# Performance work log

Measured on AMD Instinct MI355X. Metric: run time of the kernel, lower is better.

## Reference

```python
import jax, jax.numpy as jnp
import numpy as np
from jax.ops import segment_sum

N_V = 50000   # vertices
N_E = 10000   # hyperedges
N_P = 800000  # incidence pairs
D_IN = 256
D_OUT = 256
NEG_SLOPE = 0.01


def setup_inputs() -> dict:
    key = jax.random.key(0)
    k1, k2, k3, k4, k5 = jax.random.split(key, 5)
    X = jax.random.normal(k1, (N_V, D_IN), dtype=jnp.float32)
    W = jax.random.normal(k2, (D_IN, D_OUT), dtype=jnp.float32) * (1.0 / np.sqrt(D_IN))
    b = jax.random.normal(k3, (D_OUT,), dtype=jnp.float32) * 0.01
    v_idx = jax.random.randint(k4, (N_P,), 0, N_V, dtype=jnp.int32)
    e_idx = jax.random.randint(k5, (N_P,), 0, N_E, dtype=jnp.int32)
    return {"X": X, "W": W, "b": b, "v_idx": v_idx, "e_idx": e_idx,
            "num_hyperedges": N_E}


def _mean_scatter(msg, idx, num_segments):
    # segment mean with count clamped to >=1 (empty segments -> 0)
    s = segment_sum(msg, idx, num_segments=num_segments)
    cnt = segment_sum(jnp.ones((msg.shape[0],), msg.dtype), idx,
                      num_segments=num_segments)
    return s / jnp.maximum(cnt, 1.0)[:, None]


def reference(X, W, b, v_idx, e_idx, num_hyperedges):
    # theta: linear projection  [N_V, D_OUT]
    H = X @ W + b
    # v2e mean: hyperedge features from member vertices
    e_feat = _mean_scatter(H[v_idx], e_idx, num_hyperedges)   # [N_E, D_OUT]
    # e2v mean: vertex features from incident hyperedges
    v_feat = _mean_scatter(e_feat[e_idx], v_idx, X.shape[0])  # [N_V, D_OUT]
    # leaky relu, default negative slope 0.01
    return jnp.where(v_feat >= 0, v_feat, NEG_SLOPE * v_feat)
```

## Files before the change

### kernel.cpp

```cpp
#include <hip/hip_runtime.h>

#define D 256
#define NEG_SLOPE 0.01f
#define E_PAD 192
#define V_PAD 64
#define EB 32
#define VB 64
#define NBE 313
#define NBV 782
#define CAP_E 3328
#define CAP_V 1536
#define CHUNK 4096
#define NS 8
#define DS 32
#define NSE 2
#define DSE 128

__device__ __forceinline__ unsigned short f2bf(float f) {
    union { float f; unsigned u; } x; x.f = f;
    unsigned r = x.u + 0x7fffu + ((x.u >> 16) & 1u);
    return (unsigned short)(r >> 16);
}
__device__ __forceinline__ void acc8(float* acc, uint4 g) {
    union { unsigned u; float f; } t;
    t.u = g.x << 16;         acc[0] += t.f;
    t.u = g.x & 0xffff0000u; acc[1] += t.f;
    t.u = g.y << 16;         acc[2] += t.f;
    t.u = g.y & 0xffff0000u; acc[3] += t.f;
    t.u = g.z << 16;         acc[4] += t.f;
    t.u = g.z & 0xffff0000u; acc[5] += t.f;
    t.u = g.w << 16;         acc[6] += t.f;
    t.u = g.w & 0xffff0000u; acc[7] += t.f;
}

__global__ __launch_bounds__(256) void prep_kernel(
        const float* __restrict__ X, unsigned short* __restrict__ Xhs,
        const int* __restrict__ v_idx, const int* __restrict__ e_idx,
        int* __restrict__ bc_e, int* __restrict__ bc_v,
        unsigned* __restrict__ pe, unsigned* __restrict__ pv,
        int n_v, int n_p, int gp) {
    __shared__ int he[NBE], hv[NBV], beb[NBE], bvb[NBV];
    const int tid = threadIdx.x;
    if ((int)blockIdx.x < gp) {
        const int base = (int)blockIdx.x * CHUNK;
        for (int i = tid; i < NBE; i += 256) he[i] = 0;
        for (int i = tid; i < NBV; i += 256) hv[i] = 0;
        __syncthreads();
        #pragma unroll 4
        for (int r = 0; r < CHUNK / 256; ++r) {
            int p = base + r * 256 + tid;
            if (p < n_p) {
                atomicAdd(&he[e_idx[p] >> 5], 1);
                atomicAdd(&hv[v_idx[p] >> 6], 1);
            }
        }
        __syncthreads();
        for (int b = tid; b < NBE; b += 256) {
            int c = he[b];
            beb[b] = c ? atomicAdd(&bc_e[b], c) : 0;
            he[b] = 0;
        }
        for (int b = tid; b < NBV; b += 256) {
            int c = hv[b];
            bvb[b] = c ? atomicAdd(&bc_v[b], c) : 0;
            hv[b] = 0;
        }
        __syncthreads();
        #pragma unroll 4
        for (int r = 0; r < CHUNK / 256; ++r) {
            int p = base + r * 256 + tid;
            if (p < n_p) {
                int e = e_idx[p], v = v_idx[p];
                int b1 = e >> 5;
                int s1 = beb[b1] + atomicAdd(&he[b1], 1);
                if (s1 < CAP_E) pe[(size_t)b1 * CAP_E + s1] = (unsigned)v | ((unsigned)e << 16);
                int b2 = v >> 6;
                int s2 = bvb[b2] + atomicAdd(&hv[b2], 1);
                if (s2 < CAP_V) pv[(size_t)b2 * CAP_V + s2] = (unsigned)e | ((unsigned)v << 16);
            }
        }
    } else {
        int i = ((int)blockIdx.x - gp) * 256 + tid;
        if (i >= n_v * 64) return;
        int v = i >> 6;
        int d4 = (i & 63) * 4;
        float4 val = *(const float4*)(X + (size_t)v * D + d4);
        ushort4 h;
        h.x = f2bf(val.x); h.y = f2bf(val.y); h.z = f2bf(val.z); h.w = f2bf(val.w);
        int s = d4 >> 5, wd = d4 & 31;
        *(ushort4*)(Xhs + (size_t)s * n_v * DS + (size_t)v * DS + wd) = h;
    }
}

__global__ __launch_bounds__(256) void build_kernel(
        const unsigned* __restrict__ pe, const unsigned* __restrict__ pv,
        const int* __restrict__ bc_e, const int* __restrict__ bc_v,
        unsigned short* __restrict__ e_adj, int* __restrict__ e_fill,
        unsigned short* __restrict__ v_adj, int* __restrict__ v_fill,
        int n_e, int n_v) {
    __shared__ unsigned short adj[EB * E_PAD];
    __shared__ int cnt[VB];
    const int tid = threadIdx.x;
    if ((int)blockIdx.x < NBE) {
        const int b = blockIdx.x;
        const int e0 = b * EB;
        int m = n_e - e0; if (m > EB) m = EB;
        for (int i = tid; i < EB; i += 256) cnt[i] = 0;
        __syncthreads();
        int total = bc_e[b]; if (total > CAP_E) total = CAP_E;
        for (int i = tid; i < total; i += 256) {
            unsigned p = pe[(size_t)b * CAP_E + i];
            int v = (int)(p & 0xFFFFu);
            int el = (int)(p >> 16) - e0;
            int s = atomicAdd(&cnt[el], 1);
            if (s < E_PAD) adj[el * E_PAD + s] = (unsigned short)v;
        }
        __syncthreads();
        unsigned* gout = (unsigned*)(e_adj + (size_t)e0 * E_PAD);
        const unsigned* lin = (const unsigned*)adj;
        int words = m * E_PAD / 2;
        for (int j = tid; j < words; j += 256) gout[j] = lin[j];
        for (int el = tid; el < m; el += 256) {
            int c = cnt[el]; if (c > E_PAD) c = E_PAD;
            e_fill[e0 + el] = c;
        }
    } else {
        const int b = (int)blockIdx.x - NBE;
        const int v0 = b * VB;
        int m = n_v - v0; if (m > VB) m = VB;
        for (int i = tid; i < VB; i += 256) cnt[i] = 0;
        __syncthreads();
        int total = bc_v[b]; if (total > CAP_V) total = CAP_V;
        for (int i = tid; i < total; i += 256) {
            unsigned p = pv[(size_t)b * CAP_V + i];
            int e = (int)(p & 0xFFFFu);
            int vl = (int)(p >> 16) - v0;
            int s = atomicAdd(&cnt[vl], 1);
            if (s < V_PAD) adj[vl * V_PAD + s] = (unsigned short)e;
        }
        __syncthreads();
        unsigned* gout = (unsigned*)(v_adj + (size_t)v0 * V_PAD);
        const unsigned* lin = (const unsigned*)adj;
        int words = m * V_PAD / 2;
        for (int j = tid; j < words; j += 256) gout[j] = lin[j];
        for (int vl = tid; vl < m; vl += 256) {
            int c = cnt[vl]; if (c > V_PAD) c = V_PAD;
            v_fill[v0 + vl] = c;
        }
    }
}

__global__ __launch_bounds__(256) void v2e_kernel(
        const unsigned short* __restrict__ Xhs, const int* __restrict__ e_fill,
        const unsigned short* __restrict__ e_adj, float* __restrict__ Xagg,
        int n_e, int n_v) {
    const int s    = blockIdx.x;
    const int eg   = threadIdx.x >> 4;
    const int l16  = threadIdx.x & 15;
    const int ph   = l16 >> 2;
    const int sub  = l16 & 3;
    const int e    = blockIdx.y * 16 + eg;
    if (e >= n_e) return;
    const unsigned short* tab = Xhs + (size_t)s * n_v * DS + (sub << 3);
    const unsigned short* adj = e_adj + (size_t)e * E_PAD;
    int cnt = e_fill[e]; if (cnt > E_PAD) cnt = E_PAD;
    float acc[8] = {};
    int i = ph * 4;
    for (; i + 4 <= cnt; i += 16) {
        ushort4 A = *(const ushort4*)(adj + i);
        uint4 g0 = *(const uint4*)(tab + (size_t)A.x * DS);
        uint4 g1 = *(const uint4*)(tab + (size_t)A.y * DS);
        uint4 g2 = *(const uint4*)(tab + (size_t)A.z * DS);
        uint4 g3 = *(const uint4*)(tab + (size_t)A.w * DS);
        acc8(acc, g0); acc8(acc, g1); acc8(acc, g2); acc8(acc, g3);
    }
    for (int j = i; j < cnt; ++j) {
        uint4 g = *(const uint4*)(tab + (size_t)adj[j] * DS);
        acc8(acc, g);
    }
    #pragma unroll
    for (int k = 0; k < 8; ++k) {
        acc[k] += __shfl_xor(acc[k], 4);
        acc[k] += __shfl_xor(acc[k], 8);
    }
    if (ph == 0) {
        int c = cnt < 1 ? 1 : cnt;
        float inv = 1.0f / (float)c;
        float4 o0, o1;
        o0.x = acc[0] * inv; o0.y = acc[1] * inv; o0.z = acc[2] * inv; o0.w = acc[3] * inv;
        o1.x = acc[4] * inv; o1.y = acc[5] * inv; o1.z = acc[6] * inv; o1.w = acc[7] * inv;
        float* orow = Xagg + (size_t)e * D + s * DS + (sub << 3);
        *(float4*)(orow)     = o0;
        *(float4*)(orow + 4) = o1;
    }
}

#define BM 64
#define BN 64
#define BK 64
#define SAK 68
#define SBN 68

__global__ __launch_bounds__(256) void gemm_kernel(
        const float* __restrict__ A, const float* __restrict__ B,
        const float* __restrict__ bias, const int* __restrict__ e_cnt,
        unsigned short* __restrict__ Ehs, int M) {
    __shared__ float As[BM * SAK];
    __shared__ float Bs[BK * SBN];
    const int tid = threadIdx.x;
    const int tx = tid & 15, ty = tid >> 4;
    const int m0 = blockIdx.y * BM;
    const int n0 = blockIdx.x * BN;

    float acc[4][4] = {};

    for (int k0 = 0; k0 < D; k0 += BK) {
        #pragma unroll
        for (int r = 0; r < 4; ++r) {
            int l  = (tid + r * 256) * 4;
            int am = l >> 6;
            int ak = l & 63;
            int grow = m0 + am;
            float4 v = make_float4(0.f, 0.f, 0.f, 0.f);
            if (grow < M) v = *(const float4*)(A + (size_t)grow * D + k0 + ak);
            *(float4*)(&As[am * SAK + ak]) = v;
        }
        #pragma unroll
        for (int r = 0; r < 4; ++r) {
            int l  = (tid + r * 256) * 4;
            int bk = l >> 6;
            int bn = l & 63;
            float4 v = *(const float4*)(B + (size_t)(k0 + bk) * D + n0 + bn);
            *(float4*)(&Bs[bk * SBN + bn]) = v;
        }
        __syncthreads();

        #pragma unroll 8
        for (int kk = 0; kk < BK; ++kk) {
            float a0 = As[(ty * 4 + 0) * SAK + kk];
            float a1 = As[(ty * 4 + 1) * SAK + kk];
            float a2 = As[(ty * 4 + 2) * SAK + kk];
            float a3 = As[(ty * 4 + 3) * SAK + kk];
            float4 bv = *(const float4*)(Bs + kk * SBN + tx * 4);
            acc[0][0] += a0 * bv.x; acc[0][1] += a0 * bv.y; acc[0][2] += a0 * bv.z; acc[0][3] += a0 * bv.w;
            acc[1][0] += a1 * bv.x; acc[1][1] += a1 * bv.y; acc[1][2] += a1 * bv.z; acc[1][3] += a1 * bv.w;
            acc[2][0] += a2 * bv.x; acc[2][1] += a2 * bv.y; acc[2][2] += a2 * bv.z; acc[2][3] += a2 * bv.w;
            acc[3][0] += a3 * bv.x; acc[3][1] += a3 * bv.y; acc[3][2] += a3 * bv.z; acc[3][3] += a3 * bv.w;
        }
        __syncthreads();
    }

    float4 bb = *(const float4*)(bias + n0 + tx * 4);
    const int dcol = n0 + tx * 4;
    const int ss = dcol >> 7, wd = dcol & 127;
    #pragma unroll
    for (int i = 0; i < 4; ++i) {
        int row = m0 + ty * 4 + i;
        if (row < M) {
            bool nonempty = e_cnt[row] > 0;
            ushort4 o;
            o.x = f2bf(nonempty ? acc[i][0] + bb.x : 0.f);
            o.y = f2bf(nonempty ? acc[i][1] + bb.y : 0.f);
            o.z = f2bf(nonempty ? acc[i][2] + bb.z : 0.f);
            o.w = f2bf(nonempty ? acc[i][3] + bb.w : 0.f);
            *(ushort4*)(Ehs + (size_t)ss * M * DSE + (size_t)row * DSE + wd) = o;
        }
    }
}

__global__ __launch_bounds__(256) void e2v_kernel(
        const unsigned short* __restrict__ Ehs, const unsigned short* __restrict__ v_adj,
        const int* __restrict__ v_fill, float* __restrict__ out, int n_v, int n_e) {
    const int s   = blockIdx.x;
    const int grp = threadIdx.x >> 4;
    const int sub = threadIdx.x & 15;
    const int v   = blockIdx.y * 16 + grp;
    if (v >= n_v) return;
    const unsigned short* tab = Ehs + (size_t)s * n_e * DSE + (sub << 3);
    const unsigned short* a   = v_adj + (size_t)v * V_PAD;
    int c = v_fill[v]; if (c > V_PAD) c = V_PAD;
    float acc[8] = {};
    int i = 0;
    for (; i + 8 <= c; i += 8) {
        ushort4 E0 = *(const ushort4*)(a + i);
        ushort4 E1 = *(const ushort4*)(a + i + 4);
        uint4 g0 = *(const uint4*)(tab + (size_t)E0.x * DSE);
        uint4 g1 = *(const uint4*)(tab + (size_t)E0.y * DSE);
        uint4 g2 = *(const uint4*)(tab + (size_t)E0.z * DSE);
        uint4 g3 = *(const uint4*)(tab + (size_t)E0.w * DSE);
        uint4 g4 = *(const uint4*)(tab + (size_t)E1.x * DSE);
        uint4 g5 = *(const uint4*)(tab + (size_t)E1.y * DSE);
        uint4 g6 = *(const uint4*)(tab + (size_t)E1.z * DSE);
        uint4 g7 = *(const uint4*)(tab + (size_t)E1.w * DSE);
        acc8(acc, g0); acc8(acc, g1); acc8(acc, g2); acc8(acc, g3);
        acc8(acc, g4); acc8(acc, g5); acc8(acc, g6); acc8(acc, g7);
    }
    for (; i < c; ++i) {
        uint4 g = *(const uint4*)(tab + (size_t)a[i] * DSE);
        acc8(acc, g);
    }
    int cc = c < 1 ? 1 : c;
    float inv = 1.0f / (float)cc;
    float4 o0, o1;
    #pragma unroll
    for (int k = 0; k < 8; ++k) acc[k] *= inv;
    o0.x = acc[0] >= 0.f ? acc[0] : NEG_SLOPE * acc[0];
    o0.y = acc[1] >= 0.f ? acc[1] : NEG_SLOPE * acc[1];
    o0.z = acc[2] >= 0.f ? acc[2] : NEG_SLOPE * acc[2];
    o0.w = acc[3] >= 0.f ? acc[3] : NEG_SLOPE * acc[3];
    o1.x = acc[4] >= 0.f ? acc[4] : NEG_SLOPE * acc[4];
    o1.y = acc[5] >= 0.f ? acc[5] : NEG_SLOPE * acc[5];
    o1.z = acc[6] >= 0.f ? acc[6] : NEG_SLOPE * acc[6];
    o1.w = acc[7] >= 0.f ? acc[7] : NEG_SLOPE * acc[7];
    float* orow = out + (size_t)v * D + s * DSE + (sub << 3);
    *(float4*)(orow)     = o0;
    *(float4*)(orow + 4) = o1;
}

extern "C" void kernel_launch(void* const* d_in, const int* in_sizes, int n_in,
                              void* d_out, int out_size, void* d_ws, size_t ws_size,
                              hipStream_t stream) {
    const float* X    = (const float*)d_in[0];
    const float* W    = (const float*)d_in[1];
    const float* bias = (const float*)d_in[2];
    const int* v_idx  = (const int*)d_in[3];
    const int* e_idx  = (const int*)d_in[4];
    const int n_v = in_sizes[0] / D;
    const int n_p = in_sizes[3];
    const int n_e = 10000;

    char* w = (char*)d_ws;
    size_t off = 0;
    auto alloc = [&](size_t bytes) -> void* {
        void* p = w + off;
        off = (off + bytes + 255) & ~(size_t)255;
        return p;
    };
    unsigned short* Xhs = (unsigned short*)alloc((size_t)NS * n_v * DS * sizeof(unsigned short));
    float* Xagg         = (float*)alloc((size_t)n_e * D * sizeof(float));
    unsigned short* Ehs = (unsigned short*)alloc((size_t)n_e * D * sizeof(unsigned short));
    unsigned short* e_adj = (unsigned short*)alloc((size_t)n_e * E_PAD * sizeof(unsigned short));
    unsigned short* v_adj = (unsigned short*)alloc((size_t)n_v * V_PAD * sizeof(unsigned short));
    unsigned* pe   = (unsigned*)alloc((size_t)NBE * CAP_E * sizeof(unsigned));
    unsigned* pv   = (unsigned*)alloc((size_t)NBV * CAP_V * sizeof(unsigned));
    int* fills     = (int*)alloc((size_t)(n_e + n_v) * sizeof(int));
    int* e_fill = fills;
    int* v_fill = fills + n_e;
    int* bc        = (int*)alloc((size_t)(NBE + NBV) * sizeof(int));
    int* bc_e = bc;
    int* bc_v = bc + NBE;

    hipMemsetAsync(bc, 0, (size_t)(NBE + NBV) * sizeof(int), stream);

    int gp = (n_p + CHUNK - 1) / CHUNK;
    int gc = (n_v * 64 + 255) / 256;
    prep_kernel<<<gp + gc, 256, 0, stream>>>(X, Xhs, v_idx, e_idx,
                                             bc_e, bc_v, pe, pv, n_v, n_p, gp);

    build_kernel<<<NBE + NBV, 256, 0, stream>>>(pe, pv, bc_e, bc_v,
                                                e_adj, e_fill, v_adj, v_fill,
                                                n_e, n_v);

    dim3 vgrid(NS, (n_e + 15) / 16);
    v2e_kernel<<<vgrid, 256, 0, stream>>>(Xhs, e_fill, e_adj, Xagg, n_e, n_v);

    dim3 ggrid(D / BN, (n_e + BM - 1) / BM);
    gemm_kernel<<<ggrid, 256, 0, stream>>>(Xagg, W, bias, e_fill, Ehs, n_e);

    dim3 egrid(NSE, (n_v + 15) / 16);
    e2v_kernel<<<egrid, 256, 0, stream>>>(Ehs, v_adj, v_fill, (float*)d_out, n_v, n_e);
}
```

Measured before the change: 235.8 us.

## Replace global atomic bucket offsets with histogram+scan pipeline and alias workspace buffers

Splits the single prep kernel into a per-chunk histogram kernel, a per-bucket exclusive scan kernel, and a scatter kernel that reads its precomputed offsets. This drops the global atomicAdd on bucket counters and the memset, and makes bucket placement deterministic. Workspace is also aliased: pe shares memory with Xagg/Ehs and pv is placed in the output buffer, which shrinks the footprint and may improve cache locality. In exchange it adds two extra kernel launches, and the chunk count gp is silently clamped to 256, which would drop data if n_p grew.

```diff
diff --git a/kernel.cpp b/kernel.cpp
--- a/kernel.cpp
+++ b/kernel.cpp
@@ -8,9 +8,11 @@
 #define VB 64
 #define NBE 313
 #define NBV 782
+#define NBT (NBE + NBV)
 #define CAP_E 3328
 #define CAP_V 1536
 #define CHUNK 4096
+#define CR (CHUNK/256)
 #define NS 8
 #define DS 32
 #define NSE 2
@@ -33,49 +35,71 @@
     t.u = g.w & 0xffff0000u; acc[7] += t.f;
 }
 
-__global__ __launch_bounds__(256) void prep_kernel(
+__global__ __launch_bounds__(256) void hist_kernel(
+        const int* __restrict__ v_idx, const int* __restrict__ e_idx,
+        int* __restrict__ offs, int n_p, int gp) {
+    __shared__ int he[NBE], hv[NBV];
+    const int tid = threadIdx.x, blk = blockIdx.x;
+    for (int i = tid; i < NBE; i += 256) he[i] = 0;
+    for (int i = tid; i < NBV; i += 256) hv[i] = 0;
+    __syncthreads();
+    const int base = blk * CHUNK;
+    #pragma unroll 4
+    for (int r = 0; r < CR; ++r) {
+        int p = base + r * 256 + tid;
+        if (p < n_p) {
+            atomicAdd(&he[e_idx[p] >> 5], 1);
+            atomicAdd(&hv[v_idx[p] >> 6], 1);
+        }
+    }
+    __syncthreads();
+    const int g1 = gp + 1;
+    for (int b = tid; b < NBE; b += 256) offs[(size_t)b * g1 + blk] = he[b];
+    for (int b = tid; b < NBV; b += 256) offs[(size_t)(NBE + b) * g1 + blk] = hv[b];
+}
+
+__global__ __launch_bounds__(256) void scan_kernel(int* __restrict__ offs, int gp) {
+    __shared__ int sa[256], sb[256];
+    const int tid = threadIdx.x;
+    int* row = offs + (size_t)blockIdx.x * (gp + 1);
+    sa[tid] = tid < gp ? row[tid] : 0;
+    __syncthreads();
+    int *src = sa, *dst = sb;
+    for (int s = 1; s < 256; s <<= 1) {
+        int t = src[tid] + (tid >= s ? src[tid - s] : 0);
+        dst[tid] = t;
+        __syncthreads();
+        int* tmp = src; src = dst; dst = tmp;
+    }
+    if (tid < gp) row[tid] = tid ? src[tid - 1] : 0;
+    if (tid == 0) row[gp] = src[gp - 1];
+}
+
+__global__ __launch_bounds__(256) void scatter_kernel(
         const float* __restrict__ X, unsigned short* __restrict__ Xhs,
         const int* __restrict__ v_idx, const int* __restrict__ e_idx,
-        int* __restrict__ bc_e, int* __restrict__ bc_v,
+        const int* __restrict__ offs,
         unsigned* __restrict__ pe, unsigned* __restrict__ pv,
         int n_v, int n_p, int gp) {
-    __shared__ int he[NBE], hv[NBV], beb[NBE], bvb[NBV];
+    __shared__ int oe[NBE], ov[NBV], he[NBE], hv[NBV];
     const int tid = threadIdx.x;
     if ((int)blockIdx.x < gp) {
-        const int base = (int)blockIdx.x * CHUNK;
-        for (int i = tid; i < NBE; i += 256) he[i] = 0;
-        for (int i = tid; i < NBV; i += 256) hv[i] = 0;
-        __syncthreads();
+        const int blk = blockIdx.x;
+        const int g1 = gp + 1;
+        for (int b = tid; b < NBE; b += 256) { oe[b] = offs[(size_t)b * g1 + blk]; he[b] = 0; }
+        for (int b = tid; b < NBV; b += 256) { ov[b] = offs[(size_t)(NBE + b) * g1 + blk]; hv[b] = 0; }
+        __syncthreads();
+        const int base = blk * CHUNK;
         #pragma unroll 4
-        for (int r = 0; r < CHUNK / 256; ++r) {
-            int p = base + r * 256 + tid;
-            if (p < n_p) {
-                atomicAdd(&he[e_idx[p] >> 5], 1);
-                atomicAdd(&hv[v_idx[p] >> 6], 1);
-            }
-        }
-        __syncthreads();
-        for (int b = tid; b < NBE; b += 256) {
-            int c = he[b];
-            beb[b] = c ? atomicAdd(&bc_e[b], c) : 0;
-            he[b] = 0;
-        }
-        for (int b = tid; b < NBV; b += 256) {
-            int c = hv[b];
-            bvb[b] = c ? atomicAdd(&bc_v[b], c) : 0;
-            hv[b] = 0;
-        }
-        __syncthreads();
-        #pragma unroll 4
-        for (int r = 0; r < CHUNK / 256; ++r) {
+        for (int r = 0; r < CR; ++r) {
             int p = base + r * 256 + tid;
             if (p < n_p) {
                 int e = e_idx[p], v = v_idx[p];
                 int b1 = e >> 5;
-                int s1 = beb[b1] + atomicAdd(&he[b1], 1);
+                int s1 = oe[b1] + atomicAdd(&he[b1], 1);
                 if (s1 < CAP_E) pe[(size_t)b1 * CAP_E + s1] = (unsigned)v | ((unsigned)e << 16);
                 int b2 = v >> 6;
-                int s2 = bvb[b2] + atomicAdd(&hv[b2], 1);
+                int s2 = ov[b2] + atomicAdd(&hv[b2], 1);
                 if (s2 < CAP_V) pv[(size_t)b2 * CAP_V + s2] = (unsigned)e | ((unsigned)v << 16);
             }
         }
@@ -94,20 +118,21 @@
 
 __global__ __launch_bounds__(256) void build_kernel(
         const unsigned* __restrict__ pe, const unsigned* __restrict__ pv,
-        const int* __restrict__ bc_e, const int* __restrict__ bc_v,
+        const int* __restrict__ offs,
         unsigned short* __restrict__ e_adj, int* __restrict__ e_fill,
         unsigned short* __restrict__ v_adj, int* __restrict__ v_fill,
-        int n_e, int n_v) {
+        int n_e, int n_v, int gp) {
     __shared__ unsigned short adj[EB * E_PAD];
     __shared__ int cnt[VB];
     const int tid = threadIdx.x;
+    const int g1 = gp + 1;
     if ((int)blockIdx.x < NBE) {
         const int b = blockIdx.x;
         const int e0 = b * EB;
         int m = n_e - e0; if (m > EB) m = EB;
         for (int i = tid; i < EB; i += 256) cnt[i] = 0;
         __syncthreads();
-        int total = bc_e[b]; if (total > CAP_E) total = CAP_E;
+        int total = offs[(size_t)b * g1 + gp]; if (total > CAP_E) total = CAP_E;
         for (int i = tid; i < total; i += 256) {
             unsigned p = pe[(size_t)b * CAP_E + i];
             int v = (int)(p & 0xFFFFu);
@@ -130,7 +155,7 @@
         int m = n_v - v0; if (m > VB) m = VB;
         for (int i = tid; i < VB; i += 256) cnt[i] = 0;
         __syncthreads();
-        int total = bc_v[b]; if (total > CAP_V) total = CAP_V;
+        int total = offs[(size_t)(NBE + b) * g1 + gp]; if (total > CAP_V) total = CAP_V;
         for (int i = tid; i < total; i += 256) {
             unsigned p = pv[(size_t)b * CAP_V + i];
             int e = (int)(p & 0xFFFFu);
@@ -329,6 +354,9 @@
     const int n_p = in_sizes[3];
     const int n_e = 10000;
 
+    int gp = (n_p + CHUNK - 1) / CHUNK;
+    if (gp > 256) gp = 256;
+
     char* w = (char*)d_ws;
     size_t off = 0;
     auto alloc = [&](size_t bytes) -> void* {
@@ -337,29 +365,33 @@
         return p;
     };
     unsigned short* Xhs = (unsigned short*)alloc((size_t)NS * n_v * DS * sizeof(unsigned short));
-    float* Xagg         = (float*)alloc((size_t)n_e * D * sizeof(float));
-    unsigned short* Ehs = (unsigned short*)alloc((size_t)n_e * D * sizeof(unsigned short));
+    size_t pe_bytes  = (size_t)NBE * CAP_E * sizeof(unsigned);
+    size_t agg_bytes = (size_t)n_e * D * sizeof(float);
+    size_t ehs_bytes = (size_t)n_e * D * sizeof(unsigned short);
+    size_t uni_bytes = pe_bytes > agg_bytes + ehs_bytes ? pe_bytes : agg_bytes + ehs_bytes;
+    char* uni = (char*)alloc(uni_bytes);
+    unsigned* pe        = (unsigned*)uni;
+    float* Xagg         = (float*)uni;
+    unsigned short* Ehs = (unsigned short*)(uni + agg_bytes);
+    unsigned* pv        = (unsigned*)d_out;
     unsigned short* e_adj = (unsigned short*)alloc((size_t)n_e * E_PAD * sizeof(unsigned short));
     unsigned short* v_adj = (unsigned short*)alloc((size_t)n_v * V_PAD * sizeof(unsigned short));
-    unsigned* pe   = (unsigned*)alloc((size_t)NBE * CAP_E * sizeof(unsigned));
-    unsigned* pv   = (unsigned*)alloc((size_t)NBV * CAP_V * sizeof(unsigned));
+    int* offs      = (int*)alloc((size_t)NBT * (gp + 1) * sizeof(int));
     int* fills     = (int*)alloc((size_t)(n_e + n_v) * sizeof(int));
     int* e_fill = fills;
     int* v_fill = fills + n_e;
-    int* bc        = (int*)alloc((size_t)(NBE + NBV) * sizeof(int));
-    int* bc_e = bc;
-    int* bc_v = bc + NBE;
-
-    hipMemsetAsync(bc, 0, (size_t)(NBE + NBV) * sizeof(int), stream);
-
-    int gp = (n_p + CHUNK - 1) / CHUNK;
+
+    hist_kernel<<<gp, 256, 0, stream>>>(v_idx, e_idx, offs, n_p, gp);
+
+    scan_kernel<<<NBT, 256, 0, stream>>>(offs, gp);
+
     int gc = (n_v * 64 + 255) / 256;
-    prep_kernel<<<gp + gc, 256, 0, stream>>>(X, Xhs, v_idx, e_idx,
-                                             bc_e, bc_v, pe, pv, n_v, n_p, gp);
-
-    build_kernel<<<NBE + NBV, 256, 0, stream>>>(pe, pv, bc_e, bc_v,
-                                                e_adj, e_fill, v_adj, v_fill,
-                                                n_e, n_v);
+    scatter_kernel<<<gp + gc, 256, 0, stream>>>(X, Xhs, v_idx, e_idx, offs,
+                                                pe, pv, n_v, n_p, gp);
+
+    build_kernel<<<NBT, 256, 0, stream>>>(pe, pv, offs,
+                                          e_adj, e_fill, v_adj, v_fill,
+                                          n_e, n_v, gp);
 
     dim3 vgrid(NS, (n_e + 15) / 16);
     v2e_kernel<<<vgrid, 256, 0, stream>>>(Xhs, e_fill, e_adj, Xagg, n_e, n_v);
```

Measured after the change: 239.1 us. About the same (+1.4%).
